# Performance work log

Measured on AMD Instinct MI355X. Metric: run time of the kernel, lower is better.

## Reference

```python
import jax, jax.numpy as jnp
import numpy as np

EPS = 1e-06


def _phi(x):
    # elu_feature_map: elu(x) + 1  (strictly positive features)
    return jax.nn.elu(x) + 1.0


def setup_inputs() -> dict:
    key = jax.random.key(0)
    k1, k2, k3 = jax.random.split(key, 3)
    N, L, H, D = 4, 4096, 12, 64
    q = jax.random.normal(k1, (N, L, H, D), dtype=jnp.float32)
    k = jax.random.normal(k2, (N, L, H, D), dtype=jnp.float32)
    v = jax.random.normal(k3, (N, L, H, D), dtype=jnp.float32)
    return {"q": q, "k": k, "v": v}


def _causal_linear_attention(q, k, v):
    qf = _phi(q)  # [N,L,H,D]
    kf = _phi(k)
    # normalizer: z_l = q_l . (sum_{s<=l} k_s) + eps
    z = jnp.einsum('nlhd,nlhd->nlh', qf, jnp.cumsum(kf, axis=1)) + EPS
    # causal_dot_product: sequential cumulative outer-product scan over L
    q_l = jnp.moveaxis(qf, 1, 0)  # [L,N,H,D]
    k_l = jnp.moveaxis(kf, 1, 0)
    v_l = jnp.moveaxis(v, 1, 0)   # [L,N,H,M]
    N, H, D = qf.shape[0], qf.shape[2], qf.shape[3]
    M = v.shape[3]
    S0 = jnp.zeros((N, H, D, M), dtype=qf.dtype)

    def step(S, qkv):
        ql, kl, vl = qkv
        S = S + jnp.einsum('nhd,nhm->nhdm', kl, vl)  # accumulate k v^T
        o = jnp.einsum('nhd,nhdm->nhm', ql, S)       # q . S
        return S, o

    _, out = jax.lax.scan(step, S0, (q_l, k_l, v_l))  # out: [L,N,H,M]
    out = jnp.moveaxis(out, 0, 1)  # [N,L,H,M]
    return out / z[..., None]


def reference(q, k, v):
    # mask=None path of LinearAttention.forward (causal linear attention)
    return _causal_linear_attention(q, k, v)
```

## Files before the change

kernel.cpp:

```cpp
#include <hip/hip_runtime.h>


#define NBATCH 4
#define LSEQ   4096
#define NHEAD  12
#define DDIM   64
#define LSTRIDE (NHEAD * DDIM)
#define NH     (NBATCH * NHEAD)
#define EPSF   1e-6f
#define CHUNK  64
#define NUMC   (LSEQ / CHUNK)
#define PPART  32
#define CPP    (NUMC / PPART)
#define SB     72

typedef __attribute__((ext_vector_type(8))) short bf16x8;
typedef __attribute__((ext_vector_type(4))) float f32x4;

__device__ __forceinline__ float phi(float x) { return x > 0.f ? x + 1.f : __expf(x); }
__device__ __forceinline__ float4 phi4(float4 x) {
    float4 r = {phi(x.x), phi(x.y), phi(x.z), phi(x.w)};
    return r;
}

__device__ __forceinline__ unsigned short f2bf(float x) {
    union { float f; unsigned u; } v; v.f = x;
    unsigned r = v.u + 0x7fffu + ((v.u >> 16) & 1u);
    return (unsigned short)(r >> 16);
}
__device__ __forceinline__ float bf2f(short s) {
    union { float f; unsigned u; } v; v.u = ((unsigned)(unsigned short)s) << 16;
    return v.f;
}
__device__ __forceinline__ uint2 pack4(float4 a) {
    uint2 r;
    r.x = (unsigned)f2bf(a.x) | ((unsigned)f2bf(a.y) << 16);
    r.y = (unsigned)f2bf(a.z) | ((unsigned)f2bf(a.w) << 16);
    return r;
}
__device__ __forceinline__ bf16x8 packbf8(float4 a, float4 b) {
    union { bf16x8 v; uint2 u[2]; } r;
    r.u[0] = pack4(a);
    r.u[1] = pack4(b);
    return r.v;
}

__device__ __forceinline__ float4 xpose4(float4 x, int lane) {
    const bool b0 = (lane >> 4) & 1, b1 = (lane >> 5) & 1;
    float s0 = b0 ? x.x : x.y;
    float s1 = b0 ? x.z : x.w;
    s0 = __shfl_xor(s0, 16);
    s1 = __shfl_xor(s1, 16);
    float4 y;
    if (b0) { y.x = s0;  y.y = x.y; y.z = s1;  y.w = x.w; }
    else    { y.x = x.x; y.y = s0;  y.z = x.z; y.w = s1;  }
    float t0 = b1 ? y.x : y.z;
    float t1 = b1 ? y.y : y.w;
    t0 = __shfl_xor(t0, 32);
    t1 = __shfl_xor(t1, 32);
    float4 z;
    if (b1) { z.x = t0;  z.y = t1;  z.z = y.z; z.w = y.w; }
    else    { z.x = y.x; z.y = y.y; z.z = t0;  z.w = t1;  }
    return z;
}

__global__ __launch_bounds__(256) void k_psum(const float* __restrict__ kin,
                                              const float* __restrict__ vin,
                                              float* __restrict__ kvws,
                                              float* __restrict__ ksws) {
    __shared__ short sKT[64 * SB];
    __shared__ short sVT[64 * SB];
    const int b = blockIdx.x, seq = b / PPART, p = b % PPART;
    const int n0 = seq / NHEAD, h0 = seq % NHEAD;
    const int t = threadIdx.x;
    const int lane = t & 63, w = t >> 6;
    const int nn = lane & 15, qq = lane >> 4;
    const int c4 = nn << 2;

    float4 kreg[4], vreg[4];
    auto LOADKV = [&](int cc) {
        const int gb = ((n0 * LSEQ + (p * CPP + cc) * CHUNK) * NHEAD + h0) * DDIM;
#pragma unroll
        for (int rep = 0; rep < 4; ++rep) {
            const int r16 = rep * 16 + 4 * w + qq;
            kreg[rep] = *(const float4*)(kin + gb + r16 * LSTRIDE + c4);
            vreg[rep] = *(const float4*)(vin + gb + r16 * LSTRIDE + c4);
        }
    };

    f32x4 S[4] = {{0,0,0,0},{0,0,0,0},{0,0,0,0},{0,0,0,0}};
    float ks = 0.f;
    LOADKV(0);
    for (int cc = 0; cc < CPP; ++cc) {
#pragma unroll
        for (int rep = 0; rep < 4; ++rep) {
            const int l0 = rep * 16 + 4 * w;
            float4 kp = phi4(kreg[rep]);
            float4 kt = xpose4(kp, lane);
            *(uint2*)(sKT + (c4 + qq) * SB + l0) = pack4(kt);
            float4 vt = xpose4(vreg[rep], lane);
            *(uint2*)(sVT + (c4 + qq) * SB + l0) = pack4(vt);
        }
        __syncthreads();
        if (cc + 1 < CPP) LOADKV(cc + 1);
        const int rowM = 16 * w + nn;
        bf16x8 af0 = *(const bf16x8*)(sVT + rowM * SB + qq * 8);
        bf16x8 af1 = *(const bf16x8*)(sVT + rowM * SB + 32 + qq * 8);
#pragma unroll
        for (int ct = 0; ct < 4; ++ct) {
            bf16x8 bf0 = *(const bf16x8*)(sKT + (16 * ct + nn) * SB + qq * 8);
            bf16x8 bf1 = *(const bf16x8*)(sKT + (16 * ct + nn) * SB + 32 + qq * 8);
            S[ct] = __builtin_amdgcn_mfma_f32_16x16x32_bf16(af0, bf0, S[ct], 0, 0, 0);
            S[ct] = __builtin_amdgcn_mfma_f32_16x16x32_bf16(af1, bf1, S[ct], 0, 0, 0);
            if (ct == w) {
                float s = 0.f;
#pragma unroll
                for (int j = 0; j < 8; ++j) s += bf2f(bf0[j]) + bf2f(bf1[j]);
                s += __shfl_xor(s, 16);
                s += __shfl_xor(s, 32);
                ks += s;
            }
        }
        __syncthreads();
    }
    float* kvb = kvws + (size_t)b * (DDIM * DDIM);
#pragma unroll
    for (int ct = 0; ct < 4; ++ct)
#pragma unroll
        for (int r = 0; r < 4; ++r)
            kvb[(16 * w + 4 * qq + r) * DDIM + 16 * ct + nn] = S[ct][r];
    if (qq == 0) ksws[b * DDIM + 16 * w + nn] = ks;
}

__global__ __launch_bounds__(64) void k_scanP(float* __restrict__ kv,
                                              float* __restrict__ ksum) {
    const int bid = blockIdx.x;
    const int seq = bid >> 4, part16 = bid & 15;
    const int t = threadIdx.x;
    float4* base = (float4*)(kv + (size_t)seq * PPART * DDIM * DDIM) + part16 * 64 + t;
    float4 S = {0.f, 0.f, 0.f, 0.f};
    for (int b0 = 0; b0 < PPART; b0 += 8) {
        float4 x[8];
#pragma unroll
        for (int j = 0; j < 8; ++j) x[j] = base[(b0 + j) * (DDIM * DDIM / 4)];
#pragma unroll
        for (int j = 0; j < 8; ++j) {
            base[(b0 + j) * (DDIM * DDIM / 4)] = S;
            S.x += x[j].x; S.y += x[j].y; S.z += x[j].z; S.w += x[j].w;
        }
    }
    if (part16 == 0) {
        float* kb = ksum + (size_t)seq * PPART * DDIM + t;
        float s = 0.f;
        for (int b0 = 0; b0 < PPART; b0 += 8) {
            float xs[8];
#pragma unroll
            for (int j = 0; j < 8; ++j) xs[j] = kb[(b0 + j) * DDIM];
#pragma unroll
            for (int j = 0; j < 8; ++j) { kb[(b0 + j) * DDIM] = s; s += xs[j]; }
        }
    }
}

__global__ __launch_bounds__(256, 4) void k_fused(const float* __restrict__ qin,
                                                  const float* __restrict__ kin,
                                                  const float* __restrict__ vin,
                                                  const float* __restrict__ kvws,
                                                  const float* __restrict__ ksws,
                                                  float* __restrict__ out) {
    __shared__ short sK [64 * SB];
    __shared__ short sKT[64 * SB];
    __shared__ short sVT[64 * SB];
    __shared__ short sST[64 * SB];
    __shared__ float sKs[64];
    __shared__ float sZq[64];

    const int b = blockIdx.x, seq = b / PPART, p = b % PPART;
    const int n0 = seq / NHEAD, h0 = seq % NHEAD;
    const int t = threadIdx.x;
    const int lane = t & 63, w = t >> 6;
    const int nn = lane & 15, qq = lane >> 4;
    const int c4 = nn << 2;

    float4 kreg[4], vreg[4];
    auto LOADKV = [&](int cc) {
        const int gb = ((n0 * LSEQ + (p * CPP + cc) * CHUNK) * NHEAD + h0) * DDIM;
#pragma unroll
        for (int rep = 0; rep < 4; ++rep) {
            const int r16 = rep * 16 + 4 * w + qq;
            kreg[rep] = *(const float4*)(kin + gb + r16 * LSTRIDE + c4);
            vreg[rep] = *(const float4*)(vin + gb + r16 * LSTRIDE + c4);
        }
    };
    auto LOADQ = [&](int cc, bf16x8& o0, bf16x8& o1) {
        const float* qp = qin + ((n0 * LSEQ + (p * CPP + cc) * CHUNK) * NHEAD + h0) * DDIM
                        + (16 * w + nn) * LSTRIDE;
        float4 a = phi4(*(const float4*)(qp + qq * 8));
        float4 bq = phi4(*(const float4*)(qp + qq * 8 + 4));
        float4 cq = phi4(*(const float4*)(qp + 32 + qq * 8));
        float4 dq = phi4(*(const float4*)(qp + 32 + qq * 8 + 4));
        o0 = packbf8(a, bq);
        o1 = packbf8(cq, dq);
    };

    bf16x8 qf0, qf1, qfn0, qfn1;
    LOADKV(0);
    LOADQ(0, qf0, qf1);
    if (t < 64) sKs[t] = ksws[b * DDIM + t];

    const float* Sg = kvws + (size_t)b * (DDIM * DDIM);
    f32x4 Sreg[4];
#pragma unroll
    for (int ct = 0; ct < 4; ++ct) {
#pragma unroll
        for (int r = 0; r < 4; ++r) {
            const float sv = Sg[(16 * w + 4 * qq + r) * DDIM + 16 * ct + nn];
            Sreg[ct][r] = sv;
            sST[(16 * w + 4 * qq + r) * SB + 16 * ct + nn] = (short)f2bf(sv);
        }
    }

    for (int cc = 0; cc < CPP; ++cc) {
        const int gbase = ((n0 * LSEQ + (p * CPP + cc) * CHUNK) * NHEAD + h0) * DDIM;
#pragma unroll
        for (int rep = 0; rep < 4; ++rep) {
            const int row = rep * 16 + 4 * w + qq;
            const int l0 = rep * 16 + 4 * w;
            float4 kp = phi4(kreg[rep]);
            *(uint2*)(sK + row * SB + c4) = pack4(kp);
            float4 kt = xpose4(kp, lane);
            *(uint2*)(sKT + (c4 + qq) * SB + l0) = pack4(kt);
            float4 vt = xpose4(vreg[rep], lane);
            *(uint2*)(sVT + (c4 + qq) * SB + l0) = pack4(vt);
        }
        __syncthreads();

        const int rowA = 16 * w + nn;
        float am[4][4];
        float zrow[4] = {0.f, 0.f, 0.f, 0.f};
#pragma unroll
        for (int ct = 0; ct < 4; ++ct) {
            bf16x8 kf0 = *(const bf16x8*)(sK + (16 * ct + nn) * SB + qq * 8);
            bf16x8 kf1 = *(const bf16x8*)(sK + (16 * ct + nn) * SB + 32 + qq * 8);
            f32x4 acc = {0.f, 0.f, 0.f, 0.f};
            acc = __builtin_amdgcn_mfma_f32_16x16x32_bf16(qf0, kf0, acc, 0, 0, 0);
            acc = __builtin_amdgcn_mfma_f32_16x16x32_bf16(qf1, kf1, acc, 0, 0, 0);
#pragma unroll
            for (int r = 0; r < 4; ++r) {
                const int ri = 16 * w + 4 * qq + r, cj = 16 * ct + nn;
                const float mval = (cj <= ri) ? acc[r] : 0.f;
                am[ct][r] = mval;
                zrow[r] += mval;
            }
        }
#pragma unroll
        for (int r = 0; r < 4; ++r) {
            float s = zrow[r];
            s += __shfl_xor(s, 1); s += __shfl_xor(s, 2);
            s += __shfl_xor(s, 4); s += __shfl_xor(s, 8);
            zrow[r] = s;
        }
        float zq = 0.f;
#pragma unroll
        for (int j = 0; j < 8; ++j) {
            zq += bf2f(qf0[j]) * sKs[qq * 8 + j];
            zq += bf2f(qf1[j]) * sKs[32 + qq * 8 + j];
        }
        zq += __shfl_xor(zq, 16);
        zq += __shfl_xor(zq, 32);

        __syncthreads();
        if (qq == 0) sZq[16 * w + nn] = zq;
#pragma unroll
        for (int ct = 0; ct < 4; ++ct)
#pragma unroll
            for (int r = 0; r < 4; ++r)
                sK[(16 * w + 4 * qq + r) * SB + 16 * ct + nn] = (short)f2bf(am[ct][r]);
        __syncthreads();

        if (cc + 1 < CPP) {
            LOADKV(cc + 1);
            LOADQ(cc + 1, qfn0, qfn1);
        }

        f32x4 o[4] = {{0,0,0,0},{0,0,0,0},{0,0,0,0},{0,0,0,0}};
        bf16x8 af0 = *(const bf16x8*)(sK + rowA * SB + qq * 8);
        bf16x8 af1 = *(const bf16x8*)(sK + rowA * SB + 32 + qq * 8);
        bf16x8 av0 = *(const bf16x8*)(sVT + rowA * SB + qq * 8);
        bf16x8 av1 = *(const bf16x8*)(sVT + rowA * SB + 32 + qq * 8);
        float ksc = 0.f;
        __builtin_amdgcn_s_setprio(1);
#pragma unroll
        for (int ct = 0; ct < 4; ++ct) {
            bf16x8 vf0 = *(const bf16x8*)(sVT + (16 * ct + nn) * SB + qq * 8);
            bf16x8 vf1 = *(const bf16x8*)(sVT + (16 * ct + nn) * SB + 32 + qq * 8);
            o[ct] = __builtin_amdgcn_mfma_f32_16x16x32_bf16(af0, vf0, o[ct], 0, 0, 0);
            o[ct] = __builtin_amdgcn_mfma_f32_16x16x32_bf16(af1, vf1, o[ct], 0, 0, 0);
            bf16x8 sf0 = *(const bf16x8*)(sST + (16 * ct + nn) * SB + qq * 8);
            bf16x8 sf1 = *(const bf16x8*)(sST + (16 * ct + nn) * SB + 32 + qq * 8);
            o[ct] = __builtin_amdgcn_mfma_f32_16x16x32_bf16(qf0, sf0, o[ct], 0, 0, 0);
            o[ct] = __builtin_amdgcn_mfma_f32_16x16x32_bf16(qf1, sf1, o[ct], 0, 0, 0);
            bf16x8 kt0 = *(const bf16x8*)(sKT + (16 * ct + nn) * SB + qq * 8);
            bf16x8 kt1 = *(const bf16x8*)(sKT + (16 * ct + nn) * SB + 32 + qq * 8);
            Sreg[ct] = __builtin_amdgcn_mfma_f32_16x16x32_bf16(av0, kt0, Sreg[ct], 0, 0, 0);
            Sreg[ct] = __builtin_amdgcn_mfma_f32_16x16x32_bf16(av1, kt1, Sreg[ct], 0, 0, 0);
            if (ct == w) {
                float s = 0.f;
#pragma unroll
                for (int j = 0; j < 8; ++j) s += bf2f(kt0[j]) + bf2f(kt1[j]);
                s += __shfl_xor(s, 16);
                s += __shfl_xor(s, 32);
                ksc = s;
            }
        }
        __builtin_amdgcn_s_setprio(0);

#pragma unroll
        for (int r = 0; r < 4; ++r) {
            const int ri = 16 * w + 4 * qq + r;
            const float z = zrow[r] + sZq[ri] + EPSF;
            const float invz = 1.f / z;
#pragma unroll
            for (int ct = 0; ct < 4; ++ct)
                out[gbase + ri * LSTRIDE + 16 * ct + nn] = o[ct][r] * invz;
        }
        __syncthreads();
#pragma unroll
        for (int ct = 0; ct < 4; ++ct)
#pragma unroll
            for (int r = 0; r < 4; ++r)
                sST[(16 * w + 4 * qq + r) * SB + 16 * ct + nn] = (short)f2bf(Sreg[ct][r]);
        if (qq == 0) sKs[16 * w + nn] += ksc;
        qf0 = qfn0;
        qf1 = qfn1;
    }
}

__global__ __launch_bounds__(64) void k_seq(const float* __restrict__ qin,
                                            const float* __restrict__ kin,
                                            const float* __restrict__ vin,
                                            float* __restrict__ out) {
    const int seq = blockIdx.x;
    const int n = seq / NHEAD, h = seq % NHEAD;
    const int lane = threadIdx.x;
    float Scol[DDIM];
#pragma unroll
    for (int d = 0; d < DDIM; ++d) Scol[d] = 0.0f;
    float kc = 0.0f;
    __shared__ float qk[2 * DDIM];
    int base = (n * LSEQ * NHEAD + h) * DDIM + lane;
    for (int i = 0; i < LSEQ; ++i) {
        float qval = phi(qin[base]);
        float kval = phi(kin[base]);
        float vval = vin[base];
        kc += kval;
        float zp = qval * kc;
#pragma unroll
        for (int off = 32; off > 0; off >>= 1) zp += __shfl_xor(zp, off, 64);
        float z = zp + EPSF;
        qk[2 * lane] = kval;
        qk[2 * lane + 1] = qval;
        __syncthreads();
        const float4* qk4 = (const float4*)qk;
        float acc = 0.0f;
#pragma unroll
        for (int d2 = 0; d2 < DDIM / 2; ++d2) {
            float4 t0 = qk4[d2];
            int d = 2 * d2;
            Scol[d]     += t0.x * vval;  acc += t0.y * Scol[d];
            Scol[d + 1] += t0.z * vval;  acc += t0.w * Scol[d + 1];
        }
        out[base] = acc / z;
        base += LSTRIDE;
        __syncthreads();
    }
}

extern "C" void kernel_launch(void* const* d_in, const int* in_sizes, int n_in,
                              void* d_out, int out_size, void* d_ws, size_t ws_size,
                              hipStream_t stream) {
    const float* q = (const float*)d_in[0];
    const float* k = (const float*)d_in[1];
    const float* v = (const float*)d_in[2];
    float* out = (float*)d_out;
    float* ws  = (float*)d_ws;

    const size_t need = (size_t)NH * PPART * (DDIM * DDIM + DDIM) * sizeof(float);
    if (ws_size >= need) {
        float* kv   = ws;
        float* ksum = ws + (size_t)NH * PPART * DDIM * DDIM;
        k_psum <<<NH * PPART, 256, 0, stream>>>(k, v, kv, ksum);
        k_scanP<<<NH * 16,     64, 0, stream>>>(kv, ksum);
        k_fused<<<NH * PPART, 256, 0, stream>>>(q, k, v, kv, ksum, out);
    } else {
        k_seq<<<NH, 64, 0, stream>>>(q, k, v, out);
    }
}
```

Baseline: 253.2 us.

## Restructure chunked scan into local pass, prefix scan, and per-chunk fixup

```diff
diff --git a/kernel.cpp b/kernel.cpp
--- a/kernel.cpp
+++ b/kernel.cpp
@@ -10,7 +10,7 @@
 #define EPSF   1e-6f
 #define CHUNK  64
 #define NUMC   (LSEQ / CHUNK)
-#define PPART  32
+#define PPART  16
 #define CPP    (NUMC / PPART)
 #define SB     72
 
@@ -64,110 +64,13 @@
     return z;
 }
 
-__global__ __launch_bounds__(256) void k_psum(const float* __restrict__ kin,
-                                              const float* __restrict__ vin,
-                                              float* __restrict__ kvws,
-                                              float* __restrict__ ksws) {
-    __shared__ short sKT[64 * SB];
-    __shared__ short sVT[64 * SB];
-    const int b = blockIdx.x, seq = b / PPART, p = b % PPART;
-    const int n0 = seq / NHEAD, h0 = seq % NHEAD;
-    const int t = threadIdx.x;
-    const int lane = t & 63, w = t >> 6;
-    const int nn = lane & 15, qq = lane >> 4;
-    const int c4 = nn << 2;
-
-    float4 kreg[4], vreg[4];
-    auto LOADKV = [&](int cc) {
-        const int gb = ((n0 * LSEQ + (p * CPP + cc) * CHUNK) * NHEAD + h0) * DDIM;
-#pragma unroll
-        for (int rep = 0; rep < 4; ++rep) {
-            const int r16 = rep * 16 + 4 * w + qq;
-            kreg[rep] = *(const float4*)(kin + gb + r16 * LSTRIDE + c4);
-            vreg[rep] = *(const float4*)(vin + gb + r16 * LSTRIDE + c4);
-        }
-    };
-
-    f32x4 S[4] = {{0,0,0,0},{0,0,0,0},{0,0,0,0},{0,0,0,0}};
-    float ks = 0.f;
-    LOADKV(0);
-    for (int cc = 0; cc < CPP; ++cc) {
-#pragma unroll
-        for (int rep = 0; rep < 4; ++rep) {
-            const int l0 = rep * 16 + 4 * w;
-            float4 kp = phi4(kreg[rep]);
-            float4 kt = xpose4(kp, lane);
-            *(uint2*)(sKT + (c4 + qq) * SB + l0) = pack4(kt);
-            float4 vt = xpose4(vreg[rep], lane);
-            *(uint2*)(sVT + (c4 + qq) * SB + l0) = pack4(vt);
-        }
-        __syncthreads();
-        if (cc + 1 < CPP) LOADKV(cc + 1);
-        const int rowM = 16 * w + nn;
-        bf16x8 af0 = *(const bf16x8*)(sVT + rowM * SB + qq * 8);
-        bf16x8 af1 = *(const bf16x8*)(sVT + rowM * SB + 32 + qq * 8);
-#pragma unroll
-        for (int ct = 0; ct < 4; ++ct) {
-            bf16x8 bf0 = *(const bf16x8*)(sKT + (16 * ct + nn) * SB + qq * 8);
-            bf16x8 bf1 = *(const bf16x8*)(sKT + (16 * ct + nn) * SB + 32 + qq * 8);
-            S[ct] = __builtin_amdgcn_mfma_f32_16x16x32_bf16(af0, bf0, S[ct], 0, 0, 0);
-            S[ct] = __builtin_amdgcn_mfma_f32_16x16x32_bf16(af1, bf1, S[ct], 0, 0, 0);
-            if (ct == w) {
-                float s = 0.f;
-#pragma unroll
-                for (int j = 0; j < 8; ++j) s += bf2f(bf0[j]) + bf2f(bf1[j]);
-                s += __shfl_xor(s, 16);
-                s += __shfl_xor(s, 32);
-                ks += s;
-            }
-        }
-        __syncthreads();
-    }
-    float* kvb = kvws + (size_t)b * (DDIM * DDIM);
-#pragma unroll
-    for (int ct = 0; ct < 4; ++ct)
-#pragma unroll
-        for (int r = 0; r < 4; ++r)
-            kvb[(16 * w + 4 * qq + r) * DDIM + 16 * ct + nn] = S[ct][r];
-    if (qq == 0) ksws[b * DDIM + 16 * w + nn] = ks;
-}
-
-__global__ __launch_bounds__(64) void k_scanP(float* __restrict__ kv,
-                                              float* __restrict__ ksum) {
-    const int bid = blockIdx.x;
-    const int seq = bid >> 4, part16 = bid & 15;
-    const int t = threadIdx.x;
-    float4* base = (float4*)(kv + (size_t)seq * PPART * DDIM * DDIM) + part16 * 64 + t;
-    float4 S = {0.f, 0.f, 0.f, 0.f};
-    for (int b0 = 0; b0 < PPART; b0 += 8) {
-        float4 x[8];
-#pragma unroll
-        for (int j = 0; j < 8; ++j) x[j] = base[(b0 + j) * (DDIM * DDIM / 4)];
-#pragma unroll
-        for (int j = 0; j < 8; ++j) {
-            base[(b0 + j) * (DDIM * DDIM / 4)] = S;
-            S.x += x[j].x; S.y += x[j].y; S.z += x[j].z; S.w += x[j].w;
-        }
-    }
-    if (part16 == 0) {
-        float* kb = ksum + (size_t)seq * PPART * DDIM + t;
-        float s = 0.f;
-        for (int b0 = 0; b0 < PPART; b0 += 8) {
-            float xs[8];
-#pragma unroll
-            for (int j = 0; j < 8; ++j) xs[j] = kb[(b0 + j) * DDIM];
-#pragma unroll
-            for (int j = 0; j < 8; ++j) { kb[(b0 + j) * DDIM] = s; s += xs[j]; }
-        }
-    }
-}
-
-__global__ __launch_bounds__(256, 4) void k_fused(const float* __restrict__ qin,
-                                                  const float* __restrict__ kin,
-                                                  const float* __restrict__ vin,
-                                                  const float* __restrict__ kvws,
-                                                  const float* __restrict__ ksws,
-                                                  float* __restrict__ out) {
+__global__ __launch_bounds__(256) void k_pass1(const float* __restrict__ qin,
+                                               const float* __restrict__ kin,
+                                               const float* __restrict__ vin,
+                                               float* __restrict__ kvws,
+                                               float* __restrict__ ksws,
+                                               float* __restrict__ zws,
+                                               float* __restrict__ out) {
     __shared__ short sK [64 * SB];
     __shared__ short sKT[64 * SB];
     __shared__ short sVT[64 * SB];
@@ -206,19 +109,10 @@
     bf16x8 qf0, qf1, qfn0, qfn1;
     LOADKV(0);
     LOADQ(0, qf0, qf1);
-    if (t < 64) sKs[t] = ksws[b * DDIM + t];
-
-    const float* Sg = kvws + (size_t)b * (DDIM * DDIM);
-    f32x4 Sreg[4];
-#pragma unroll
-    for (int ct = 0; ct < 4; ++ct) {
-#pragma unroll
-        for (int r = 0; r < 4; ++r) {
-            const float sv = Sg[(16 * w + 4 * qq + r) * DDIM + 16 * ct + nn];
-            Sreg[ct][r] = sv;
-            sST[(16 * w + 4 * qq + r) * SB + 16 * ct + nn] = (short)f2bf(sv);
-        }
-    }
+    if (t < 64) sKs[t] = 0.f;
+
+    f32x4 Sreg[4] = {{0,0,0,0},{0,0,0,0},{0,0,0,0},{0,0,0,0}};
+    float ksTot = 0.f;
 
     for (int cc = 0; cc < CPP; ++cc) {
         const int gbase = ((n0 * LSEQ + (p * CPP + cc) * CHUNK) * NHEAD + h0) * DDIM;
@@ -261,13 +155,15 @@
             zrow[r] = s;
         }
         float zq = 0.f;
-#pragma unroll
-        for (int j = 0; j < 8; ++j) {
-            zq += bf2f(qf0[j]) * sKs[qq * 8 + j];
-            zq += bf2f(qf1[j]) * sKs[32 + qq * 8 + j];
-        }
-        zq += __shfl_xor(zq, 16);
-        zq += __shfl_xor(zq, 32);
+        if (cc) {
+#pragma unroll
+            for (int j = 0; j < 8; ++j) {
+                zq += bf2f(qf0[j]) * sKs[qq * 8 + j];
+                zq += bf2f(qf1[j]) * sKs[32 + qq * 8 + j];
+            }
+            zq += __shfl_xor(zq, 16);
+            zq += __shfl_xor(zq, 32);
+        }
 
         __syncthreads();
         if (qq == 0) sZq[16 * w + nn] = zq;
@@ -289,17 +185,18 @@
         bf16x8 av0 = *(const bf16x8*)(sVT + rowA * SB + qq * 8);
         bf16x8 av1 = *(const bf16x8*)(sVT + rowA * SB + 32 + qq * 8);
         float ksc = 0.f;
-        __builtin_amdgcn_s_setprio(1);
 #pragma unroll
         for (int ct = 0; ct < 4; ++ct) {
             bf16x8 vf0 = *(const bf16x8*)(sVT + (16 * ct + nn) * SB + qq * 8);
             bf16x8 vf1 = *(const bf16x8*)(sVT + (16 * ct + nn) * SB + 32 + qq * 8);
             o[ct] = __builtin_amdgcn_mfma_f32_16x16x32_bf16(af0, vf0, o[ct], 0, 0, 0);
             o[ct] = __builtin_amdgcn_mfma_f32_16x16x32_bf16(af1, vf1, o[ct], 0, 0, 0);
-            bf16x8 sf0 = *(const bf16x8*)(sST + (16 * ct + nn) * SB + qq * 8);
-            bf16x8 sf1 = *(const bf16x8*)(sST + (16 * ct + nn) * SB + 32 + qq * 8);
-            o[ct] = __builtin_amdgcn_mfma_f32_16x16x32_bf16(qf0, sf0, o[ct], 0, 0, 0);
-            o[ct] = __builtin_amdgcn_mfma_f32_16x16x32_bf16(qf1, sf1, o[ct], 0, 0, 0);
+            if (cc) {
+                bf16x8 sf0 = *(const bf16x8*)(sST + (16 * ct + nn) * SB + qq * 8);
+                bf16x8 sf1 = *(const bf16x8*)(sST + (16 * ct + nn) * SB + 32 + qq * 8);
+                o[ct] = __builtin_amdgcn_mfma_f32_16x16x32_bf16(qf0, sf0, o[ct], 0, 0, 0);
+                o[ct] = __builtin_amdgcn_mfma_f32_16x16x32_bf16(qf1, sf1, o[ct], 0, 0, 0);
+            }
             bf16x8 kt0 = *(const bf16x8*)(sKT + (16 * ct + nn) * SB + qq * 8);
             bf16x8 kt1 = *(const bf16x8*)(sKT + (16 * ct + nn) * SB + 32 + qq * 8);
             Sreg[ct] = __builtin_amdgcn_mfma_f32_16x16x32_bf16(av0, kt0, Sreg[ct], 0, 0, 0);
@@ -313,26 +210,140 @@
                 ksc = s;
             }
         }
-        __builtin_amdgcn_s_setprio(0);
+        ksTot += ksc;
 
 #pragma unroll
         for (int r = 0; r < 4; ++r) {
             const int ri = 16 * w + 4 * qq + r;
-            const float z = zrow[r] + sZq[ri] + EPSF;
-            const float invz = 1.f / z;
+            if (nn == 0)
+                zws[seq * LSEQ + (p * CPP + cc) * CHUNK + ri] = zrow[r] + sZq[ri];
 #pragma unroll
             for (int ct = 0; ct < 4; ++ct)
-                out[gbase + ri * LSTRIDE + 16 * ct + nn] = o[ct][r] * invz;
-        }
-        __syncthreads();
+                out[gbase + ri * LSTRIDE + 16 * ct + nn] = o[ct][r];
+        }
+        __syncthreads();
+        if (cc + 1 < CPP) {
+#pragma unroll
+            for (int ct = 0; ct < 4; ++ct)
+#pragma unroll
+                for (int r = 0; r < 4; ++r)
+                    sST[(16 * w + 4 * qq + r) * SB + 16 * ct + nn] = (short)f2bf(Sreg[ct][r]);
+            if (qq == 0) sKs[16 * w + nn] += ksc;
+            qf0 = qfn0;
+            qf1 = qfn1;
+        }
+    }
+
+    float* kvb = kvws + (size_t)b * (DDIM * DDIM);
+#pragma unroll
+    for (int ct = 0; ct < 4; ++ct)
+#pragma unroll
+        for (int r = 0; r < 4; ++r)
+            kvb[(16 * w + 4 * qq + r) * DDIM + 16 * ct + nn] = Sreg[ct][r];
+    if (qq == 0) ksws[b * DDIM + 16 * w + nn] = ksTot;
+}
+
+__global__ __launch_bounds__(64) void k_scanP(float* __restrict__ kv,
+                                              float* __restrict__ ksum) {
+    const int bid = blockIdx.x;
+    const int seq = bid >> 4, part = bid & 15;
+    const int t = threadIdx.x;
+    float4* base = (float4*)(kv + (size_t)seq * PPART * DDIM * DDIM) + part * 64 + t;
+    float4 x[PPART];
+#pragma unroll
+    for (int c = 0; c < PPART; ++c) x[c] = base[c * (DDIM * DDIM / 4)];
+    float4 S = {0.f, 0.f, 0.f, 0.f};
+#pragma unroll
+    for (int c = 0; c < PPART; ++c) {
+        base[c * (DDIM * DDIM / 4)] = S;
+        S.x += x[c].x; S.y += x[c].y; S.z += x[c].z; S.w += x[c].w;
+    }
+    if (part == 0) {
+        float* kb = ksum + (size_t)seq * PPART * DDIM + t;
+        float xs[PPART];
+#pragma unroll
+        for (int c = 0; c < PPART; ++c) xs[c] = kb[c * DDIM];
+        float s = 0.f;
+#pragma unroll
+        for (int c = 0; c < PPART; ++c) { kb[c * DDIM] = s; s += xs[c]; }
+    }
+}
+
+__global__ __launch_bounds__(256) void k_fix(const float* __restrict__ qin,
+                                             const float* __restrict__ kvws,
+                                             const float* __restrict__ ksws,
+                                             const float* __restrict__ zws,
+                                             float* __restrict__ out) {
+    __shared__ short sST[64 * SB];
+    __shared__ float sKs[64];
+    __shared__ float sZq[64];
+
+    const int cg = blockIdx.x;
+    const int seq = cg / NUMC, c = cg % NUMC, p = c / CPP;
+    const int n0 = seq / NHEAD, h0 = seq % NHEAD;
+    const int t = threadIdx.x;
+    const int lane = t & 63, w = t >> 6;
+    const int nn = lane & 15, qq = lane >> 4;
+    const int c4 = nn << 2;
+    const int gbase = ((n0 * LSEQ + c * CHUNK) * NHEAD + h0) * DDIM;
+
+    if (t < 64) sKs[t] = ksws[(seq * PPART + p) * DDIM + t];
+
+    const float* Sg = kvws + (size_t)(seq * PPART + p) * (DDIM * DDIM);
+#pragma unroll
+    for (int rep = 0; rep < 4; ++rep) {
+        const int row = rep * 16 + 4 * w + qq;
+        float4 sv = *(const float4*)(Sg + row * DDIM + c4);
+        *(uint2*)(sST + row * SB + c4) = pack4(sv);
+    }
+
+    const float* qp = qin + gbase + (16 * w + nn) * LSTRIDE;
+    float4 a  = phi4(*(const float4*)(qp + qq * 8));
+    float4 bq = phi4(*(const float4*)(qp + qq * 8 + 4));
+    float4 cq = phi4(*(const float4*)(qp + 32 + qq * 8));
+    float4 dq = phi4(*(const float4*)(qp + 32 + qq * 8 + 4));
+    bf16x8 qf0 = packbf8(a, bq);
+    bf16x8 qf1 = packbf8(cq, dq);
+
+    f32x4 o[4];
+    float zl[4];
+#pragma unroll
+    for (int r = 0; r < 4; ++r) {
+        const int ri = 16 * w + 4 * qq + r;
+        zl[r] = zws[seq * LSEQ + c * CHUNK + ri];
 #pragma unroll
         for (int ct = 0; ct < 4; ++ct)
-#pragma unroll
-            for (int r = 0; r < 4; ++r)
-                sST[(16 * w + 4 * qq + r) * SB + 16 * ct + nn] = (short)f2bf(Sreg[ct][r]);
-        if (qq == 0) sKs[16 * w + nn] += ksc;
-        qf0 = qfn0;
-        qf1 = qfn1;
+            o[ct][r] = out[gbase + ri * LSTRIDE + 16 * ct + nn];
+    }
+    __syncthreads();
+
+    float zq = 0.f;
+#pragma unroll
+    for (int j = 0; j < 8; ++j) {
+        zq += bf2f(qf0[j]) * sKs[qq * 8 + j];
+        zq += bf2f(qf1[j]) * sKs[32 + qq * 8 + j];
+    }
+    zq += __shfl_xor(zq, 16);
+    zq += __shfl_xor(zq, 32);
+    if (qq == 0) sZq[16 * w + nn] = zq;
+
+#pragma unroll
+    for (int ct = 0; ct < 4; ++ct) {
+        bf16x8 sf0 = *(const bf16x8*)(sST + (16 * ct + nn) * SB + qq * 8);
+        bf16x8 sf1 = *(const bf16x8*)(sST + (16 * ct + nn) * SB + 32 + qq * 8);
+        o[ct] = __builtin_amdgcn_mfma_f32_16x16x32_bf16(qf0, sf0, o[ct], 0, 0, 0);
+        o[ct] = __builtin_amdgcn_mfma_f32_16x16x32_bf16(qf1, sf1, o[ct], 0, 0, 0);
+    }
+    __syncthreads();
+
+#pragma unroll
+    for (int r = 0; r < 4; ++r) {
+        const int ri = 16 * w + 4 * qq + r;
+        const float z = zl[r] + sZq[ri] + EPSF;
+        const float invz = 1.f / z;
+#pragma unroll
+        for (int ct = 0; ct < 4; ++ct)
+            out[gbase + ri * LSTRIDE + 16 * ct + nn] = o[ct][r] * invz;
     }
 }
 
@@ -385,13 +396,15 @@
     float* out = (float*)d_out;
     float* ws  = (float*)d_ws;
 
-    const size_t need = (size_t)NH * PPART * (DDIM * DDIM + DDIM) * sizeof(float);
+    const size_t need = ((size_t)NH * PPART * (DDIM * DDIM + DDIM)
+                        + (size_t)NH * LSEQ) * sizeof(float);
     if (ws_size >= need) {
         float* kv   = ws;
-        float* ksum = ws + (size_t)NH * PPART * DDIM * DDIM;
-        k_psum <<<NH * PPART, 256, 0, stream>>>(k, v, kv, ksum);
+        float* ksum = kv + (size_t)NH * PPART * DDIM * DDIM;
+        float* zws  = ksum + (size_t)NH * PPART * DDIM;
+        k_pass1<<<NH * PPART, 256, 0, stream>>>(q, k, v, kv, ksum, zws, out);
         k_scanP<<<NH * 16,     64, 0, stream>>>(kv, ksum);
-        k_fused<<<NH * PPART, 256, 0, stream>>>(q, k, v, kv, ksum, out);
+        k_fix  <<<NH * NUMC,  256, 0, stream>>>(q, kv, ksum, zws, out);
     } else {
         k_seq<<<NH, 64, 0, stream>>>(q, k, v, out);
     }
```

New measurement: 220.2 us. -13.0%, faster.

## Keep masked attention tile in registers via transposed MFMA, halve partitions

Applied to the files above, without the earlier changes.

```diff
diff --git a/kernel.cpp b/kernel.cpp
--- a/kernel.cpp
+++ b/kernel.cpp
@@ -10,7 +10,7 @@
 #define EPSF   1e-6f
 #define CHUNK  64
 #define NUMC   (LSEQ / CHUNK)
-#define PPART  32
+#define PPART  16
 #define CPP    (NUMC / PPART)
 #define SB     72
 
@@ -23,6 +23,11 @@
     return r;
 }
 
+__device__ __forceinline__ unsigned cvt2(float lo, float hi) {
+    unsigned r;
+    asm("v_cvt_pk_bf16_f32 %0, %1, %2" : "=v"(r) : "v"(lo), "v"(hi));
+    return r;
+}
 __device__ __forceinline__ unsigned short f2bf(float x) {
     union { float f; unsigned u; } v; v.f = x;
     unsigned r = v.u + 0x7fffu + ((v.u >> 16) & 1u);
@@ -34,8 +39,8 @@
 }
 __device__ __forceinline__ uint2 pack4(float4 a) {
     uint2 r;
-    r.x = (unsigned)f2bf(a.x) | ((unsigned)f2bf(a.y) << 16);
-    r.y = (unsigned)f2bf(a.z) | ((unsigned)f2bf(a.w) << 16);
+    r.x = cvt2(a.x, a.y);
+    r.y = cvt2(a.z, a.w);
     return r;
 }
 __device__ __forceinline__ bf16x8 packbf8(float4 a, float4 b) {
@@ -64,6 +69,15 @@
     return z;
 }
 
+__device__ __forceinline__ void swapbit(uint2& A, uint2& B, int m, bool hi) {
+    uint2 t;
+    t.x = hi ? A.x : B.x;
+    t.y = hi ? A.y : B.y;
+    t.x = (unsigned)__shfl_xor((int)t.x, m);
+    t.y = (unsigned)__shfl_xor((int)t.y, m);
+    if (hi) { A.x = t.x; A.y = t.y; } else { B.x = t.x; B.y = t.y; }
+}
+
 __global__ __launch_bounds__(256) void k_psum(const float* __restrict__ kin,
                                               const float* __restrict__ vin,
                                               float* __restrict__ kvws,
@@ -135,45 +149,40 @@
 __global__ __launch_bounds__(64) void k_scanP(float* __restrict__ kv,
                                               float* __restrict__ ksum) {
     const int bid = blockIdx.x;
-    const int seq = bid >> 4, part16 = bid & 15;
+    const int seq = bid >> 4, part = bid & 15;
     const int t = threadIdx.x;
-    float4* base = (float4*)(kv + (size_t)seq * PPART * DDIM * DDIM) + part16 * 64 + t;
+    float4* base = (float4*)(kv + (size_t)seq * PPART * DDIM * DDIM) + part * 64 + t;
+    float4 x[PPART];
+#pragma unroll
+    for (int c = 0; c < PPART; ++c) x[c] = base[c * (DDIM * DDIM / 4)];
     float4 S = {0.f, 0.f, 0.f, 0.f};
-    for (int b0 = 0; b0 < PPART; b0 += 8) {
-        float4 x[8];
-#pragma unroll
-        for (int j = 0; j < 8; ++j) x[j] = base[(b0 + j) * (DDIM * DDIM / 4)];
-#pragma unroll
-        for (int j = 0; j < 8; ++j) {
-            base[(b0 + j) * (DDIM * DDIM / 4)] = S;
-            S.x += x[j].x; S.y += x[j].y; S.z += x[j].z; S.w += x[j].w;
-        }
-    }
-    if (part16 == 0) {
+#pragma unroll
+    for (int c = 0; c < PPART; ++c) {
+        base[c * (DDIM * DDIM / 4)] = S;
+        S.x += x[c].x; S.y += x[c].y; S.z += x[c].z; S.w += x[c].w;
+    }
+    if (part == 0) {
         float* kb = ksum + (size_t)seq * PPART * DDIM + t;
+        float xs[PPART];
+#pragma unroll
+        for (int c = 0; c < PPART; ++c) xs[c] = kb[c * DDIM];
         float s = 0.f;
-        for (int b0 = 0; b0 < PPART; b0 += 8) {
-            float xs[8];
-#pragma unroll
-            for (int j = 0; j < 8; ++j) xs[j] = kb[(b0 + j) * DDIM];
-#pragma unroll
-            for (int j = 0; j < 8; ++j) { kb[(b0 + j) * DDIM] = s; s += xs[j]; }
-        }
-    }
-}
-
-__global__ __launch_bounds__(256, 4) void k_fused(const float* __restrict__ qin,
-                                                  const float* __restrict__ kin,
-                                                  const float* __restrict__ vin,
-                                                  const float* __restrict__ kvws,
-                                                  const float* __restrict__ ksws,
-                                                  float* __restrict__ out) {
+#pragma unroll
+        for (int c = 0; c < PPART; ++c) { kb[c * DDIM] = s; s += xs[c]; }
+    }
+}
+
+__global__ __launch_bounds__(256) void k_fused(const float* __restrict__ qin,
+                                               const float* __restrict__ kin,
+                                               const float* __restrict__ vin,
+                                               const float* __restrict__ kvws,
+                                               const float* __restrict__ ksws,
+                                               float* __restrict__ out) {
     __shared__ short sK [64 * SB];
     __shared__ short sKT[64 * SB];
     __shared__ short sVT[64 * SB];
     __shared__ short sST[64 * SB];
     __shared__ float sKs[64];
-    __shared__ float sZq[64];
 
     const int b = blockIdx.x, seq = b / PPART, p = b % PPART;
     const int n0 = seq / NHEAD, h0 = seq % NHEAD;
@@ -181,6 +190,8 @@
     const int lane = t & 63, w = t >> 6;
     const int nn = lane & 15, qq = lane >> 4;
     const int c4 = nn << 2;
+    const bool b4 = (lane >> 4) & 1, b5 = (lane >> 5) & 1;
+    const int iRow = 16 * w + nn;
 
     float4 kreg[4], vreg[4];
     auto LOADKV = [&](int cc) {
@@ -194,7 +205,7 @@
     };
     auto LOADQ = [&](int cc, bf16x8& o0, bf16x8& o1) {
         const float* qp = qin + ((n0 * LSEQ + (p * CPP + cc) * CHUNK) * NHEAD + h0) * DDIM
-                        + (16 * w + nn) * LSTRIDE;
+                        + iRow * LSTRIDE;
         float4 a = phi4(*(const float4*)(qp + qq * 8));
         float4 bq = phi4(*(const float4*)(qp + qq * 8 + 4));
         float4 cq = phi4(*(const float4*)(qp + 32 + qq * 8));
@@ -235,71 +246,68 @@
         }
         __syncthreads();
 
-        const int rowA = 16 * w + nn;
-        float am[4][4];
-        float zrow[4] = {0.f, 0.f, 0.f, 0.f};
+        if (cc + 1 < CPP) {
+            LOADKV(cc + 1);
+            LOADQ(cc + 1, qfn0, qfn1);
+        }
+
+        uint2 W[4];
+        float zpart = 0.f;
 #pragma unroll
         for (int ct = 0; ct < 4; ++ct) {
             bf16x8 kf0 = *(const bf16x8*)(sK + (16 * ct + nn) * SB + qq * 8);
             bf16x8 kf1 = *(const bf16x8*)(sK + (16 * ct + nn) * SB + 32 + qq * 8);
             f32x4 acc = {0.f, 0.f, 0.f, 0.f};
-            acc = __builtin_amdgcn_mfma_f32_16x16x32_bf16(qf0, kf0, acc, 0, 0, 0);
-            acc = __builtin_amdgcn_mfma_f32_16x16x32_bf16(qf1, kf1, acc, 0, 0, 0);
-#pragma unroll
-            for (int r = 0; r < 4; ++r) {
-                const int ri = 16 * w + 4 * qq + r, cj = 16 * ct + nn;
-                const float mval = (cj <= ri) ? acc[r] : 0.f;
-                am[ct][r] = mval;
-                zrow[r] += mval;
+            acc = __builtin_amdgcn_mfma_f32_16x16x32_bf16(kf0, qf0, acc, 0, 0, 0);
+            acc = __builtin_amdgcn_mfma_f32_16x16x32_bf16(kf1, qf1, acc, 0, 0, 0);
+            float4 mv;
+            mv.x = (16 * ct + 4 * qq + 0 <= iRow) ? acc[0] : 0.f;
+            mv.y = (16 * ct + 4 * qq + 1 <= iRow) ? acc[1] : 0.f;
+            mv.z = (16 * ct + 4 * qq + 2 <= iRow) ? acc[2] : 0.f;
+            mv.w = (16 * ct + 4 * qq + 3 <= iRow) ? acc[3] : 0.f;
+            zpart += mv.x + mv.y + mv.z + mv.w;
+            W[ct] = pack4(mv);
+        }
+        zpart += __shfl_xor(zpart, 16);
+        zpart += __shfl_xor(zpart, 32);
+        float zi = zpart;
+        {
+            float zq = 0.f;
+#pragma unroll
+            for (int j = 0; j < 8; ++j) {
+                zq += bf2f(qf0[j]) * sKs[qq * 8 + j];
+                zq += bf2f(qf1[j]) * sKs[32 + qq * 8 + j];
             }
-        }
-#pragma unroll
-        for (int r = 0; r < 4; ++r) {
-            float s = zrow[r];
-            s += __shfl_xor(s, 1); s += __shfl_xor(s, 2);
-            s += __shfl_xor(s, 4); s += __shfl_xor(s, 8);
-            zrow[r] = s;
-        }
-        float zq = 0.f;
-#pragma unroll
-        for (int j = 0; j < 8; ++j) {
-            zq += bf2f(qf0[j]) * sKs[qq * 8 + j];
-            zq += bf2f(qf1[j]) * sKs[32 + qq * 8 + j];
-        }
-        zq += __shfl_xor(zq, 16);
-        zq += __shfl_xor(zq, 32);
-
-        __syncthreads();
-        if (qq == 0) sZq[16 * w + nn] = zq;
-#pragma unroll
-        for (int ct = 0; ct < 4; ++ct)
-#pragma unroll
-            for (int r = 0; r < 4; ++r)
-                sK[(16 * w + 4 * qq + r) * SB + 16 * ct + nn] = (short)f2bf(am[ct][r]);
-        __syncthreads();
-
-        if (cc + 1 < CPP) {
-            LOADKV(cc + 1);
-            LOADQ(cc + 1, qfn0, qfn1);
-        }
+            zq += __shfl_xor(zq, 16);
+            zq += __shfl_xor(zq, 32);
+            zi += zq;
+        }
+
+        swapbit(W[0], W[1], 32, b5);
+        swapbit(W[2], W[3], 32, b5);
+        swapbit(W[0], W[1], 16, b4);
+        swapbit(W[2], W[3], 16, b4);
+        union U8 { unsigned u[4]; bf16x8 v; };
+        U8 a0, a1;
+        a0.u[0] = W[0].x; a0.u[1] = W[0].y; a0.u[2] = W[1].x; a0.u[3] = W[1].y;
+        a1.u[0] = W[2].x; a1.u[1] = W[2].y; a1.u[2] = W[3].x; a1.u[3] = W[3].y;
+        const bf16x8 amB0 = a0.v;
+        const bf16x8 amB1 = a1.v;
 
         f32x4 o[4] = {{0,0,0,0},{0,0,0,0},{0,0,0,0},{0,0,0,0}};
-        bf16x8 af0 = *(const bf16x8*)(sK + rowA * SB + qq * 8);
-        bf16x8 af1 = *(const bf16x8*)(sK + rowA * SB + 32 + qq * 8);
-        bf16x8 av0 = *(const bf16x8*)(sVT + rowA * SB + qq * 8);
-        bf16x8 av1 = *(const bf16x8*)(sVT + rowA * SB + 32 + qq * 8);
+        bf16x8 av0 = *(const bf16x8*)(sVT + iRow * SB + qq * 8);
+        bf16x8 av1 = *(const bf16x8*)(sVT + iRow * SB + 32 + qq * 8);
         float ksc = 0.f;
-        __builtin_amdgcn_s_setprio(1);
 #pragma unroll
         for (int ct = 0; ct < 4; ++ct) {
             bf16x8 vf0 = *(const bf16x8*)(sVT + (16 * ct + nn) * SB + qq * 8);
             bf16x8 vf1 = *(const bf16x8*)(sVT + (16 * ct + nn) * SB + 32 + qq * 8);
-            o[ct] = __builtin_amdgcn_mfma_f32_16x16x32_bf16(af0, vf0, o[ct], 0, 0, 0);
-            o[ct] = __builtin_amdgcn_mfma_f32_16x16x32_bf16(af1, vf1, o[ct], 0, 0, 0);
+            o[ct] = __builtin_amdgcn_mfma_f32_16x16x32_bf16(vf0, amB0, o[ct], 0, 0, 0);
+            o[ct] = __builtin_amdgcn_mfma_f32_16x16x32_bf16(vf1, amB1, o[ct], 0, 0, 0);
             bf16x8 sf0 = *(const bf16x8*)(sST + (16 * ct + nn) * SB + qq * 8);
             bf16x8 sf1 = *(const bf16x8*)(sST + (16 * ct + nn) * SB + 32 + qq * 8);
-            o[ct] = __builtin_amdgcn_mfma_f32_16x16x32_bf16(qf0, sf0, o[ct], 0, 0, 0);
-            o[ct] = __builtin_amdgcn_mfma_f32_16x16x32_bf16(qf1, sf1, o[ct], 0, 0, 0);
+            o[ct] = __builtin_amdgcn_mfma_f32_16x16x32_bf16(sf0, qf0, o[ct], 0, 0, 0);
+            o[ct] = __builtin_amdgcn_mfma_f32_16x16x32_bf16(sf1, qf1, o[ct], 0, 0, 0);
             bf16x8 kt0 = *(const bf16x8*)(sKT + (16 * ct + nn) * SB + qq * 8);
             bf16x8 kt1 = *(const bf16x8*)(sKT + (16 * ct + nn) * SB + 32 + qq * 8);
             Sreg[ct] = __builtin_amdgcn_mfma_f32_16x16x32_bf16(av0, kt0, Sreg[ct], 0, 0, 0);
@@ -313,26 +321,27 @@
                 ksc = s;
             }
         }
-        __builtin_amdgcn_s_setprio(0);
-
-#pragma unroll
-        for (int r = 0; r < 4; ++r) {
-            const int ri = 16 * w + 4 * qq + r;
-            const float z = zrow[r] + sZq[ri] + EPSF;
-            const float invz = 1.f / z;
+
+        const float invz = 1.f / (zi + EPSF);
+        float* orow = out + gbase + iRow * LSTRIDE;
+#pragma unroll
+        for (int ct = 0; ct < 4; ++ct) {
+            f32x4 r = o[ct];
+            r[0] *= invz; r[1] *= invz; r[2] *= invz; r[3] *= invz;
+            *(f32x4*)(orow + 16 * ct + 4 * qq) = r;
+        }
+
+        __syncthreads();
+        if (cc + 1 < CPP) {
 #pragma unroll
             for (int ct = 0; ct < 4; ++ct)
-                out[gbase + ri * LSTRIDE + 16 * ct + nn] = o[ct][r] * invz;
-        }
-        __syncthreads();
-#pragma unroll
-        for (int ct = 0; ct < 4; ++ct)
-#pragma unroll
-            for (int r = 0; r < 4; ++r)
-                sST[(16 * w + 4 * qq + r) * SB + 16 * ct + nn] = (short)f2bf(Sreg[ct][r]);
-        if (qq == 0) sKs[16 * w + nn] += ksc;
-        qf0 = qfn0;
-        qf1 = qfn1;
+#pragma unroll
+                for (int r = 0; r < 4; ++r)
+                    sST[(16 * w + 4 * qq + r) * SB + 16 * ct + nn] = (short)f2bf(Sreg[ct][r]);
+            if (qq == 0) sKs[16 * w + nn] += ksc;
+            qf0 = qfn0;
+            qf1 = qfn1;
+        }
     }
 }
 
```

Result: faster. 203.2 us (-19.8%).
